# Kernel tuning notes

Hardware: AMD Instinct MI355X
Metric: run time of the kernel (lower is better)

## Reference

```python
import jax, jax.numpy as jnp
import numpy as np

COMMITMENT_COST = 0.25
NUM_EMBEDDINGS = 512
EMBEDDING_DIM = 128


def setup_inputs() -> dict:
    key = jax.random.key(0)
    k1, k2 = jax.random.split(key)
    z = jax.random.normal(k1, (64, 128, 32, 32), dtype=jnp.float32)
    # nn.Embedding weight initialized uniform(-1/K, 1/K)
    lim = 1.0 / NUM_EMBEDDINGS
    emb_weight = jax.random.uniform(
        k2, (NUM_EMBEDDINGS, EMBEDDING_DIM), dtype=jnp.float32,
        minval=-lim, maxval=lim)
    return {"z": z, "emb_weight": emb_weight}


def reference(z, emb_weight):
    b, c, h, w = z.shape  # c == embedding_dim
    # (b, h, w, c) -> (b*h*w, c)
    z_cl = jnp.transpose(z, (0, 2, 3, 1))
    z_flat = z_cl.reshape(b * h * w, c)
    # squared L2 distances: ||z||^2 + ||e||^2 - 2 z.e  -> [N, K]
    distances = (
        jnp.sum(z_flat ** 2, axis=-1, keepdims=True)
        + jnp.sum(emb_weight ** 2, axis=-1)[None, :]
        - 2.0 * jnp.matmul(z_flat, emb_weight.T)
    )
    encoding_indices = jnp.argmin(distances, axis=-1)  # [N]
    z_q = emb_weight[encoding_indices]                 # [N, c]
    z_q = z_q.reshape(b, h, w, c)
    z_q = jnp.transpose(z_q, (0, 3, 1, 2))             # [b, c, h, w]
    loss = (
        jnp.mean((z_q - jax.lax.stop_gradient(z)) ** 2)
        + COMMITMENT_COST * jnp.mean((jax.lax.stop_gradient(z_q) - z) ** 2)
    )
    # straight-through estimator
    z_q_st = z + jax.lax.stop_gradient(z_q - z)
    return (z_q_st, loss, encoding_indices)
```

## Files before the change

kernel.cpp:

```cpp
#include <hip/hip_runtime.h>


#define D_DIM 128
#define HW    1024
#define GAP_THR 4e-4f
#define FLAG_CAP 16384

typedef short short8 __attribute__((ext_vector_type(8)));
typedef float f32x16 __attribute__((ext_vector_type(16)));

union U8 { unsigned int u[4]; short8 s; uint4 q; };

__device__ __forceinline__ unsigned short f2bf(float v) {
    unsigned int u = __builtin_bit_cast(unsigned int, v);
    return (unsigned short)((u + 0x7fffu + ((u >> 16) & 1u)) >> 16);
}
__device__ __forceinline__ unsigned int umn(unsigned int a, unsigned int b) {
    return a < b ? a : b;
}
__device__ __forceinline__ unsigned int umx(unsigned int a, unsigned int b) {
    return a > b ? a : b;
}

__global__ void prep_kernel(const float* __restrict__ emb,
                            float* __restrict__ etr,
                            uint4* __restrict__ ebh,
                            float* __restrict__ se) {
    const int t = blockIdx.x * 256 + threadIdx.x;

    {
        const int k = t >> 7;
        const int d = t & 127;
        etr[d * 512 + k] = emb[t];
    }

    if (t < 8192) {
        const int lane = t & 63;
        const int ks   = (t >> 6) & 7;
        const int kcol = t >> 9;
        const int krow = kcol * 32 + (lane & 31);
        const int d0   = ks * 16 + (lane >> 5) * 8;
        const float* ep = emb + (size_t)krow * D_DIM + d0;
        float v[8];
        #pragma unroll
        for (int j = 0; j < 8; ++j) v[j] = ep[j];
        U8 hh;
        #pragma unroll
        for (int p = 0; p < 4; ++p) {
            const unsigned short h0 = f2bf(v[2*p]), h1 = f2bf(v[2*p+1]);
            hh.u[p] = (unsigned int)h0 | ((unsigned int)h1 << 16);
        }
        ebh[t] = hh.q;
    }

    if (t < 512) {
        const float* e = emb + (size_t)t * D_DIM;
        float r[8];
        #pragma unroll
        for (int j = 0; j < 8; ++j) {
            float v = e[j];
            float p = v * v;
            asm("" : "+v"(p));
            r[j] = p;
        }
        for (int i = 8; i < 128; i += 8) {
            #pragma unroll
            for (int j = 0; j < 8; ++j) {
                float v = e[i + j];
                float p = v * v;
                asm("" : "+v"(p));
                r[j] += p;
            }
        }
        se[t] = ((r[0] + r[1]) + (r[2] + r[3])) + ((r[4] + r[5]) + (r[6] + r[7]));
    }
}

__launch_bounds__(256, 4)
__global__ void dist_kernel(const float* __restrict__ z,
                            const uint4* __restrict__ ebh,
                            const float* __restrict__ se_g,
                            const float* __restrict__ emb,
                            float* __restrict__ idx_out,
                            unsigned int* __restrict__ flag_cnt,
                            int* __restrict__ flag_list,
                            float* __restrict__ zq,
                            double* __restrict__ loss) {
    __shared__ unsigned int red1[2][64], red2[2][64];
    __shared__ int   li_sh[64];
    __shared__ float ept[D_DIM * 33];
    __shared__ float lred[4];

    const int tid  = threadIdx.x;
    const int lane = tid & 63;
    const int wid  = tid >> 6;
    const int wn   = wid >> 1;
    const int wk   = wid & 1;
    const int row  = lane & 31;
    const int bidl = (int)blockIdx.x;
    const int bid  = (bidl & 7) * 128 + (bidl >> 3);
    const int nblk = bid * 64;
    const int bimg = nblk >> 10;
    const int hw0  = nblk & 1023;
    const int hww  = hw0 + wn * 32;

    short8 Ah[8];
    {
        const float* zc = z + (size_t)bimg * (D_DIM * HW) + hww + row;
        #pragma unroll
        for (int ks = 0; ks < 8; ++ks) {
            const int d0 = ks * 16 + (lane >> 5) * 8;
            float v[8];
            #pragma unroll
            for (int j = 0; j < 8; ++j) v[j] = zc[(size_t)(d0 + j) * HW];
            U8 hh;
            #pragma unroll
            for (int p = 0; p < 4; ++p) {
                unsigned int hwd;
                asm("v_cvt_pk_bf16_f32 %0, %1, %2" : "=v"(hwd) : "v"(v[2*p]), "v"(v[2*p+1]));
                hh.u[p] = hwd;
            }
            Ah[ks] = hh.s;
        }
    }

    unsigned int b1[16], b2[16];
    #pragma unroll
    for (int j = 0; j < 16; ++j) { b1[j] = 0xFFFFFFFFu; b2[j] = 0xFFFFFFFFu; }

    for (int i = 0; i < 8; ++i) {
        const int   kc   = wk * 8 + ((i + bidl) & 7);
        const int   kgl  = kc * 32 + row;
        const float sevp = se_g[kgl] + 0.5f;
        const uint4* pbh = ebh + kc * 512 + lane;

        f32x16 acc;
        #pragma unroll
        for (int j = 0; j < 16; ++j) acc[j] = 0.f;

        __builtin_amdgcn_s_setprio(1);
        #pragma unroll
        for (int ks = 0; ks < 8; ++ks) {
            U8 bh; bh.q = pbh[ks * 64];
            acc = __builtin_amdgcn_mfma_f32_32x32x16_bf16(Ah[ks], bh.s, acc, 0, 0, 0);
        }
        __builtin_amdgcn_s_setprio(0);

        #pragma unroll
        for (int j = 0; j < 16; ++j) {
            const float pd = fmaf(-2.f, acc[j], sevp);
            const unsigned int key =
                (__builtin_bit_cast(unsigned int, pd) & 0xFFFFFE00u) | (unsigned int)kgl;
            const unsigned int m = umn(key, b1[j]);
            b2[j] = umn(umx(key, b1[j]), b2[j]);
            b1[j] = m;
        }
    }

    #pragma unroll
    for (int off = 1; off <= 16; off <<= 1) {
        #pragma unroll
        for (int j = 0; j < 16; ++j) {
            const unsigned int o1 = (unsigned int)__shfl_xor((int)b1[j], off);
            const unsigned int o2 = (unsigned int)__shfl_xor((int)b2[j], off);
            const unsigned int m  = umn(b1[j], o1);
            b2[j] = umn(umx(b1[j], o1), umn(b2[j], o2));
            b1[j] = m;
        }
    }

    if ((lane & 31) == 0) {
        const int half = lane >> 5;
        #pragma unroll
        for (int j = 0; j < 16; ++j) {
            const int r = wn * 32 + (j & 3) + 8 * (j >> 2) + 4 * half;
            red1[wk][r] = b1[j];
            red2[wk][r] = b2[j];
        }
    }
    __syncthreads();

    if (tid < 64) {
        const unsigned int v1a = red1[0][tid], v2a = red2[0][tid];
        const unsigned int v1b = red1[1][tid], v2b = red2[1][tid];
        const unsigned int m1 = umn(v1a, v1b);
        const unsigned int m2 = umn(umn(v2a, v2b), umx(v1a, v1b));
        const int n = nblk + tid;
        const int code = (int)(m1 & 511u);
        idx_out[n] = (float)code;
        li_sh[tid] = code;
        const float f1 = __builtin_bit_cast(float, m1 & 0xFFFFFE00u);
        const float f2 = __builtin_bit_cast(float, m2 & 0xFFFFFE00u);
        if (f2 - f1 < GAP_THR) {
            unsigned int p = atomicAdd(flag_cnt, 1u);
            if (p < FLAG_CAP) flag_list[p] = n;
        }
    }

    float lacc = 0.f;
    for (int h = 0; h < 2; ++h) {
        __syncthreads();
        {
            const int p   = tid >> 3;
            const int sub = tid & 7;
            const float* er = emb + (size_t)li_sh[h * 32 + p] * D_DIM + sub * 16;
            #pragma unroll
            for (int j4 = 0; j4 < 4; ++j4) {
                const float4 v = *(const float4*)(er + j4 * 4);
                const int c = sub * 16 + j4 * 4;
                ept[(c + 0) * 33 + p] = v.x;
                ept[(c + 1) * 33 + p] = v.y;
                ept[(c + 2) * 33 + p] = v.z;
                ept[(c + 3) * 33 + p] = v.w;
            }
        }
        __syncthreads();
        {
            const int p  = tid & 31;
            const int c0 = tid >> 5;
            const int hwp = hw0 + h * 32 + p;
            const float* zb2 = z  + (size_t)bimg * (D_DIM * HW) + hwp;
            float*       qb  = zq + (size_t)bimg * (D_DIM * HW) + hwp;
            #pragma unroll
            for (int i = 0; i < 16; ++i) {
                const int c = c0 + i * 8;
                const float v  = ept[c * 33 + p];
                const float zv = zb2[(size_t)c * HW];
                qb[(size_t)c * HW] = v;
                const float df = v - zv;
                lacc = fmaf(df, df, lacc);
            }
        }
    }
    #pragma unroll
    for (int off = 32; off > 0; off >>= 1) lacc += __shfl_down(lacc, off);
    if (lane == 0) lred[wid] = lacc;
    __syncthreads();
    if (tid == 0)
        atomicAdd(loss, (double)(lred[0] + lred[1] + lred[2] + lred[3]));
}

__launch_bounds__(512)
__global__ void fixup_kernel(const float* __restrict__ z,
                             const float* __restrict__ etr,
                             const unsigned int* __restrict__ flag_cnt,
                             const int* __restrict__ flag_list,
                             const float* __restrict__ se_np,
                             float* __restrict__ idx_out) {
    __shared__ float zrow[D_DIM];
    __shared__ float q[D_DIM];
    __shared__ float rsum[8];
    __shared__ float szs;
    __shared__ float rv[8];
    __shared__ int   rix[8];

    const int tid = threadIdx.x;
    unsigned int cnt = *flag_cnt;
    if (cnt > FLAG_CAP) cnt = FLAG_CAP;

    for (unsigned int f = blockIdx.x; f < cnt; f += gridDim.x) {
        const int row = flag_list[f];
        const int b   = row >> 10;
        const int hw  = row & 1023;
        __syncthreads();
        if (tid < D_DIM) {
            float v = z[(size_t)b * (D_DIM * HW) + (size_t)tid * HW + hw];
            zrow[tid] = v;
            q[tid] = v * v;
        }
        __syncthreads();
        if (tid < 8) {
            float r = q[tid];
            for (int i = 8; i < 128; i += 8) r += q[i + tid];
            rsum[tid] = r;
        }
        __syncthreads();
        if (tid == 0)
            szs = ((rsum[0] + rsum[1]) + (rsum[2] + rsum[3]))
                + ((rsum[4] + rsum[5]) + (rsum[6] + rsum[7]));
        __syncthreads();
        const float sz32 = szs;

        const int k = tid;
        double dot0 = 0.0, dot1 = 0.0;
        #pragma unroll 4
        for (int d = 0; d < D_DIM; d += 2) {
            dot0 += (double)etr[d * 512 + k]       * (double)zrow[d];
            dot1 += (double)etr[(d + 1) * 512 + k] * (double)zrow[d + 1];
        }
        const float dotf = (float)(dot0 + dot1);
        const float T    = sz32 + se_np[k];
        float best  = T - 2.0f * dotf;
        int   besti = k;

        #pragma unroll
        for (int off = 32; off > 0; off >>= 1) {
            const float ov = __shfl_down(best, off);
            const int   oi = __shfl_down(besti, off);
            if (ov < best || (ov == best && oi < besti)) { best = ov; besti = oi; }
        }
        if ((tid & 63) == 0) { rv[tid >> 6] = best; rix[tid >> 6] = besti; }
        __syncthreads();
        if (tid == 0) {
            #pragma unroll
            for (int w = 1; w < 8; ++w)
                if (rv[w] < best || (rv[w] == best && rix[w] < besti)) {
                    best = rv[w]; besti = rix[w];
                }
            idx_out[row] = (float)besti;
        }
    }
}

__global__ void fin_kernel(const double* __restrict__ loss, float* __restrict__ out_loss) {
    *out_loss = (float)(*loss * 1.25 / 8388608.0);
}

extern "C" void kernel_launch(void* const* d_in, const int* in_sizes, int n_in,
                              void* d_out, int out_size, void* d_ws, size_t ws_size,
                              hipStream_t stream) {
    const float* z   = (const float*)d_in[0];
    const float* emb = (const float*)d_in[1];
    float* out      = (float*)d_out;
    float* zq       = out;
    float* out_loss = out + 8388608;
    float* idx_f    = out + 8388609;

    char* ws = (char*)d_ws;
    unsigned int* flag_cnt = (unsigned int*)ws;
    double*       loss     = (double*)(ws + 8);
    float*        se       = (float*)(ws + 10240);
    uint4*        ebh      = (uint4*)(ws + 16384);
    int*          flag_list= (int*)(ws + 16384 + 262144);
    float*        etr      = (float*)(ws + 16384 + 262144 + 65536);

    hipMemsetAsync(d_ws, 0, 16384, stream);
    prep_kernel <<<256,  256, 0, stream>>>(emb, etr, ebh, se);
    dist_kernel <<<1024, 256, 0, stream>>>(z, ebh, se, emb, idx_f,
                                           flag_cnt, flag_list, zq, loss);
    fixup_kernel<<<2048, 512, 0, stream>>>(z, etr, flag_cnt, flag_list, se, idx_f);
    fin_kernel  <<<1,    1,   0, stream>>>(loss, out_loss);
}
```

Measured before the change: 98.89 us.

## Double-buffer codebook tile loads in registers ahead of MFMA chunks

```diff
diff --git a/kernel.cpp b/kernel.cpp
--- a/kernel.cpp
+++ b/kernel.cpp
@@ -76,7 +76,7 @@
     }
 }
 
-__launch_bounds__(256, 4)
+__launch_bounds__(256, 3)
 __global__ void dist_kernel(const float* __restrict__ z,
                             const uint4* __restrict__ ebh,
                             const float* __restrict__ se_g,
@@ -128,32 +128,76 @@
     #pragma unroll
     for (int j = 0; j < 16; ++j) { b1[j] = 0xFFFFFFFFu; b2[j] = 0xFFFFFFFFu; }
 
+    int kcs[8];
+    float sevp[8];
+    #pragma unroll
     for (int i = 0; i < 8; ++i) {
-        const int   kc   = wk * 8 + ((i + bidl) & 7);
-        const int   kgl  = kc * 32 + row;
-        const float sevp = se_g[kgl] + 0.5f;
-        const uint4* pbh = ebh + kc * 512 + lane;
-
-        f32x16 acc;
-        #pragma unroll
-        for (int j = 0; j < 16; ++j) acc[j] = 0.f;
-
-        __builtin_amdgcn_s_setprio(1);
-        #pragma unroll
-        for (int ks = 0; ks < 8; ++ks) {
-            U8 bh; bh.q = pbh[ks * 64];
-            acc = __builtin_amdgcn_mfma_f32_32x32x16_bf16(Ah[ks], bh.s, acc, 0, 0, 0);
-        }
-        __builtin_amdgcn_s_setprio(0);
-
-        #pragma unroll
-        for (int j = 0; j < 16; ++j) {
-            const float pd = fmaf(-2.f, acc[j], sevp);
-            const unsigned int key =
-                (__builtin_bit_cast(unsigned int, pd) & 0xFFFFFE00u) | (unsigned int)kgl;
-            const unsigned int m = umn(key, b1[j]);
-            b2[j] = umn(umx(key, b1[j]), b2[j]);
-            b1[j] = m;
+        kcs[i]  = wk * 8 + ((i + bidl) & 7);
+        sevp[i] = se_g[kcs[i] * 32 + row] + 0.5f;
+    }
+
+    uint4 B0[8], B1[8];
+    {
+        const uint4* p0 = ebh + kcs[0] * 512 + lane;
+        #pragma unroll
+        for (int ks = 0; ks < 8; ++ks) B0[ks] = p0[ks * 64];
+    }
+
+    #pragma unroll
+    for (int i = 0; i < 8; i += 2) {
+        if (i + 1 < 8) {
+            const uint4* pn = ebh + kcs[i + 1] * 512 + lane;
+            #pragma unroll
+            for (int ks = 0; ks < 8; ++ks) B1[ks] = pn[ks * 64];
+        }
+        {
+            f32x16 acc;
+            #pragma unroll
+            for (int j = 0; j < 16; ++j) acc[j] = 0.f;
+            __builtin_amdgcn_s_setprio(1);
+            #pragma unroll
+            for (int ks = 0; ks < 8; ++ks) {
+                U8 bh; bh.q = B0[ks];
+                acc = __builtin_amdgcn_mfma_f32_32x32x16_bf16(Ah[ks], bh.s, acc, 0, 0, 0);
+            }
+            __builtin_amdgcn_s_setprio(0);
+            const int kgl = kcs[i] * 32 + row;
+            #pragma unroll
+            for (int j = 0; j < 16; ++j) {
+                const float pd = fmaf(-2.f, acc[j], sevp[i]);
+                const unsigned int key =
+                    (__builtin_bit_cast(unsigned int, pd) & 0xFFFFFE00u) | (unsigned int)kgl;
+                const unsigned int m = umn(key, b1[j]);
+                b2[j] = umn(umx(key, b1[j]), b2[j]);
+                b1[j] = m;
+            }
+        }
+        if (i + 2 < 8) {
+            const uint4* pn = ebh + kcs[i + 2] * 512 + lane;
+            #pragma unroll
+            for (int ks = 0; ks < 8; ++ks) B0[ks] = pn[ks * 64];
+        }
+        {
+            f32x16 acc;
+            #pragma unroll
+            for (int j = 0; j < 16; ++j) acc[j] = 0.f;
+            __builtin_amdgcn_s_setprio(1);
+            #pragma unroll
+            for (int ks = 0; ks < 8; ++ks) {
+                U8 bh; bh.q = B1[ks];
+                acc = __builtin_amdgcn_mfma_f32_32x32x16_bf16(Ah[ks], bh.s, acc, 0, 0, 0);
+            }
+            __builtin_amdgcn_s_setprio(0);
+            const int kgl = kcs[i + 1] * 32 + row;
+            #pragma unroll
+            for (int j = 0; j < 16; ++j) {
+                const float pd = fmaf(-2.f, acc[j], sevp[i + 1]);
+                const unsigned int key =
+                    (__builtin_bit_cast(unsigned int, pd) & 0xFFFFFE00u) | (unsigned int)kgl;
+                const unsigned int m = umn(key, b1[j]);
+                b2[j] = umn(umx(key, b1[j]), b2[j]);
+                b1[j] = m;
+            }
         }
     }
 
```

Result: slower. 112.1 us (+13.4%).
